# Performance work log

Hardware: AMD Instinct MI355X
Metric: run time of the kernel (lower is better)

The kernel has to match this reference:

```python
import jax, jax.numpy as jnp
import numpy as np

B, N, C, H, W = 2, 2048, 1024, 16, 8  # batch, seq, dim, heads, band half-width
HD = C // H
SCALE = HD ** -0.5


def band_mask(n, w):
    # rows i: allowed cols lo..hi inclusive, matching get_attn_mask
    i = jnp.arange(n)[:, None]
    j = jnp.arange(n)[None, :]
    lo = jnp.where(i <= w, 0, i - w)
    hi = jnp.where(n - i <= w, n - 1, i + w)
    return (j >= lo) & (j <= hi)  # [N, N] bool


def setup_inputs() -> dict:
    key = jax.random.key(0)
    k1, k2, k3 = jax.random.split(key, 3)
    x = jax.random.normal(k1, (B, N, C), dtype=jnp.float32)
    Wqkv = jax.random.normal(k2, (C, 3 * C), dtype=jnp.float32) * (C ** -0.5)
    Wproj = jax.random.normal(k3, (C, C), dtype=jnp.float32) * (C ** -0.5)
    bproj = jnp.zeros((C,), dtype=jnp.float32)
    return {"x": x, "Wqkv": Wqkv, "Wproj": Wproj, "bproj": bproj}


def reference(x, Wqkv, Wproj, bproj):
    b, n, c = x.shape
    qkv = (x @ Wqkv).reshape(b, n, 3, H, HD)
    qkv = jnp.transpose(qkv, (2, 0, 3, 1, 4))  # [3, B, H, N, HD]
    q, k, v = qkv[0], qkv[1], qkv[2]
    attn = jnp.einsum('bhqd,bhkd->bhqk', q, k) * SCALE
    mask = band_mask(n, W)  # [N, N]
    attn = jnp.where(mask[None, None], attn, jnp.float32(-1e9))
    attn = jax.nn.softmax(attn, axis=-1)
    # dropout omitted (eval mode / deterministic reference)
    out = jnp.einsum('bhqk,bhkd->bhqd', attn, v)
    out = jnp.transpose(out, (0, 2, 1, 3)).reshape(b, n, c)
    return out @ Wproj + bproj
```

## Files before the change

### kernel.cpp

```cpp
#include <hip/hip_runtime.h>

typedef unsigned short ushort_t;
typedef unsigned int uint32;

typedef __bf16 bf16x8 __attribute__((ext_vector_type(8)));
typedef float f32x4 __attribute__((ext_vector_type(4)));

__device__ __forceinline__ uint32 f2bf1(float f) {
  uint32 b = __float_as_uint(f);
  return (b + 0x7FFFu + ((b >> 16) & 1u)) >> 16;
}
__device__ __forceinline__ uint32 packbf2(float a, float b) {
  return f2bf1(a) | (f2bf1(b) << 16);
}
__device__ __forceinline__ float bflo(uint32 u) { return __uint_as_float(u << 16); }
__device__ __forceinline__ float bfhi(uint32 u) { return __uint_as_float(u & 0xFFFF0000u); }

__device__ __forceinline__ void gload16(const void* g, void* l) {
  __builtin_amdgcn_global_load_lds(
      (const __attribute__((address_space(1))) unsigned int*)g,
      (__attribute__((address_space(3))) unsigned int*)l, 16, 0, 0);
}

__global__ __launch_bounds__(256) void prep_inputs(
    const float* __restrict__ x, ushort_t* __restrict__ xb,
    const float* __restrict__ Wqkv, ushort_t* __restrict__ wqkvT,
    const float* __restrict__ Wproj, ushort_t* __restrict__ wprT) {
  int bx = blockIdx.x;
  const int tid = threadIdx.x;
  if (bx < 4096) {
    const int i = bx * 256 + tid;
    float4 v = ((const float4*)x)[i];
    uint2 r;
    r.x = packbf2(v.x, v.y);
    r.y = packbf2(v.z, v.w);
    ((uint2*)xb)[i] = r;
    return;
  }
  bx -= 4096;
  const int gx = bx & 127, gy = bx >> 7;
  __shared__ float tile[32][33];
  const int tx = tid & 31, ty = tid >> 5;
  const float* src;
  ushort_t* dst;
  int Cc, c0;
  if (gx < 96) { src = Wqkv;  dst = wqkvT; Cc = 3072; c0 = gx << 5; }
  else         { src = Wproj; dst = wprT;  Cc = 1024; c0 = (gx - 96) << 5; }
  const int r0 = gy << 5;
#pragma unroll
  for (int i = 0; i < 4; ++i)
    tile[ty + i * 8][tx] = src[(size_t)(r0 + ty + i * 8) * Cc + c0 + tx];
  __syncthreads();
#pragma unroll
  for (int i = 0; i < 4; ++i)
    dst[(size_t)(c0 + ty + i * 8) * 1024 + r0 + tx] = (ushort_t)f2bf1(tile[tx][ty + i * 8]);
}


template <int ROWS>
__device__ __forceinline__ void stage2(ushort_t* dst, const ushort_t* gbase,
                                       int ldK, int tid) {
  const int r = tid >> 2, s = tid & 3;
  const int c = ((s ^ ((r >> 1) & 3)) << 3);
  const int wvb = (tid >> 6) << 9;
  const ushort_t* g = gbase + (size_t)r * ldK + c;
  gload16(g, dst + wvb);
  if (ROWS == 128) gload16(g + (size_t)64 * ldK, dst + 2048 + wvb);
}

template <bool OUT_BF16, int MF, int NF>
__global__ __launch_bounds__(256) void gemm2p(
    const ushort_t* __restrict__ A, const ushort_t* __restrict__ Bt,
    void* __restrict__ Cout, const float* __restrict__ bias,
    const int M, const int Nn, const int K) {
  constexpr int BM = MF * 32, BN = NF * 32;
  constexpr int AL = BM * 32, BL = BN * 32;
  __shared__ ushort_t lA[2 * AL];
  __shared__ ushort_t lB[2 * BL];
  const int tid = threadIdx.x;
  const int lane = tid & 63, wave = tid >> 6;
  const int wm = wave >> 1, wn = wave & 1;

  const int nwg = gridDim.x * gridDim.y;
  const int wg0 = blockIdx.y * gridDim.x + blockIdx.x;
  const int q8 = nwg >> 3;
  const int wg = (wg0 & 7) * q8 + (wg0 >> 3);
  const int bm = (wg / gridDim.x) * BM;
  const int bn = (wg % gridDim.x) * BN;

  const int l15 = lane & 15, l16 = lane >> 4;
  const int cK = ((l16 ^ ((l15 >> 1) & 3)) << 3);

  const ushort_t* gA = A + (size_t)bm * K;
  const ushort_t* gB = Bt + (size_t)bn * K;

  f32x4 acc[MF][NF] = {};

  stage2<BM>(lA, gA, K, tid);
  stage2<BN>(lB, gB, K, tid);
  __syncthreads();

  int buf = 0;
  for (int k0 = 0; k0 < K; k0 += 32) {
    if (k0 + 32 < K) {
      stage2<BM>(lA + (buf ^ 1) * AL, gA + k0 + 32, K, tid);
      stage2<BN>(lB + (buf ^ 1) * BL, gB + k0 + 32, K, tid);
    }
    bf16x8 a[MF], b[NF];
#pragma unroll
    for (int m = 0; m < MF; ++m)
      a[m] = *(const bf16x8*)&lA[buf * AL + ((wm * MF + m) * 16 + l15) * 32 + cK];
#pragma unroll
    for (int n = 0; n < NF; ++n)
      b[n] = *(const bf16x8*)&lB[buf * BL + ((wn * NF + n) * 16 + l15) * 32 + cK];
#pragma unroll
    for (int m = 0; m < MF; ++m)
#pragma unroll
      for (int n = 0; n < NF; ++n)
        acc[m][n] = __builtin_amdgcn_mfma_f32_16x16x32_bf16(a[m], b[n], acc[m][n], 0, 0, 0);
    __syncthreads();
    buf ^= 1;
  }

  const int r0 = bm + wm * (MF * 16) + (l16 << 2);
  const int c0 = bn + wn * (NF * 16) + l15;
#pragma unroll
  for (int m = 0; m < MF; ++m)
#pragma unroll
    for (int n = 0; n < NF; ++n)
#pragma unroll
      for (int j = 0; j < 4; ++j) {
        const int row = r0 + m * 16 + j;
        const int col = c0 + n * 16;
        if (OUT_BF16)
          ((ushort_t*)Cout)[(size_t)row * Nn + col] = (ushort_t)f2bf1(acc[m][n][j]);
        else
          ((float*)Cout)[(size_t)row * Nn + col] = acc[m][n][j] + bias[col];
      }
}

__global__ __launch_bounds__(256) void attn_band(
    const ushort_t* __restrict__ qkv, ushort_t* __restrict__ aout) {
  __shared__ float Ks[80 * 68];
  __shared__ float Vs[80 * 68];
  const int tid = threadIdx.x;
  const int i0 = blockIdx.x << 6;
  const int h = blockIdx.y;
  const int b = blockIdx.z;
  const size_t rowbase = (size_t)b * 2048;

  for (int idx = tid; idx < 1280; idx += 256) {
    const int t = idx >> 4, c = idx & 15;
    const int j = i0 - 8 + t;
    float k0 = 0.f, k1 = 0.f, k2 = 0.f, k3 = 0.f;
    float v0 = 0.f, v1 = 0.f, v2 = 0.f, v3 = 0.f;
    if ((unsigned)j < 2048u) {
      const ushort_t* p = qkv + (rowbase + j) * 3072 + (h << 6) + (c << 2);
      uint2 rk = *(const uint2*)(p + 1024);
      uint2 rv = *(const uint2*)(p + 2048);
      k0 = bflo(rk.x); k1 = bfhi(rk.x); k2 = bflo(rk.y); k3 = bfhi(rk.y);
      v0 = bflo(rv.x); v1 = bfhi(rv.x); v2 = bflo(rv.y); v3 = bfhi(rv.y);
    }
    *(float4*)&Ks[t * 68 + (c << 2)] = make_float4(k0, k1, k2, k3);
    *(float4*)&Vs[t * 68 + (c << 2)] = make_float4(v0, v1, v2, v3);
  }
  __syncthreads();

  const int lane = tid & 63, wv = tid >> 6;
  const int qs = lane >> 2, dg = lane & 3;
  const int qi = (wv << 4) + qs;
  const int i = i0 + qi;

  const ushort_t* qp = qkv + (rowbase + i) * 3072 + (h << 6) + (dg << 4);
  float q[16];
  {
    uint4 u0 = *(const uint4*)qp;
    uint4 u1 = *(const uint4*)(qp + 8);
    q[0] = bflo(u0.x); q[1] = bfhi(u0.x); q[2] = bflo(u0.y); q[3] = bfhi(u0.y);
    q[4] = bflo(u0.z); q[5] = bfhi(u0.z); q[6] = bflo(u0.w); q[7] = bfhi(u0.w);
    q[8] = bflo(u1.x); q[9] = bfhi(u1.x); q[10] = bflo(u1.y); q[11] = bfhi(u1.y);
    q[12] = bflo(u1.z); q[13] = bfhi(u1.z); q[14] = bflo(u1.w); q[15] = bfhi(u1.w);
  }

  float s[17];
#pragma unroll
  for (int jo = 0; jo < 17; ++jo) {
    const float* kr = &Ks[(qi + jo) * 68 + (dg << 4)];
    float d = 0.f;
#pragma unroll
    for (int c = 0; c < 4; ++c) {
      float4 kv = *(const float4*)(kr + (c << 2));
      d += q[c * 4 + 0] * kv.x + q[c * 4 + 1] * kv.y +
           q[c * 4 + 2] * kv.z + q[c * 4 + 3] * kv.w;
    }
    d += __shfl_xor(d, 1);
    d += __shfl_xor(d, 2);
    const int jg = i - 8 + jo;
    s[jo] = ((unsigned)jg < 2048u) ? d * 0.125f : -1e30f;
  }
  float m = s[0];
#pragma unroll
  for (int jo = 1; jo < 17; ++jo) m = fmaxf(m, s[jo]);
  float sum = 0.f;
#pragma unroll
  for (int jo = 0; jo < 17; ++jo) {
    s[jo] = __expf(s[jo] - m);
    sum += s[jo];
  }
  const float inv = 1.f / sum;

  float o[16];
#pragma unroll
  for (int dd = 0; dd < 16; ++dd) o[dd] = 0.f;
#pragma unroll
  for (int jo = 0; jo < 17; ++jo) {
    const float* vr = &Vs[(qi + jo) * 68 + (dg << 4)];
    const float w = s[jo];
#pragma unroll
    for (int c = 0; c < 4; ++c) {
      float4 vv = *(const float4*)(vr + (c << 2));
      o[c * 4 + 0] += w * vv.x; o[c * 4 + 1] += w * vv.y;
      o[c * 4 + 2] += w * vv.z; o[c * 4 + 3] += w * vv.w;
    }
  }

  ushort_t* op = aout + (rowbase + i) * 1024 + (h << 6) + (dg << 4);
  uint4 w0, w1;
  w0.x = packbf2(o[0] * inv, o[1] * inv);
  w0.y = packbf2(o[2] * inv, o[3] * inv);
  w0.z = packbf2(o[4] * inv, o[5] * inv);
  w0.w = packbf2(o[6] * inv, o[7] * inv);
  w1.x = packbf2(o[8] * inv, o[9] * inv);
  w1.y = packbf2(o[10] * inv, o[11] * inv);
  w1.z = packbf2(o[12] * inv, o[13] * inv);
  w1.w = packbf2(o[14] * inv, o[15] * inv);
  *(uint4*)op = w0;
  *(uint4*)(op + 8) = w1;
}

extern "C" void kernel_launch(void* const* d_in, const int* in_sizes, int n_in,
                              void* d_out, int out_size, void* d_ws, size_t ws_size,
                              hipStream_t stream) {
  const float* x = (const float*)d_in[0];
  const float* Wqkv = (const float*)d_in[1];
  const float* Wproj = (const float*)d_in[2];
  const float* bproj = (const float*)d_in[3];
  float* out = (float*)d_out;

  char* ws = (char*)d_ws;
  ushort_t* xb    = (ushort_t*)(ws);
  ushort_t* wqkvT = (ushort_t*)(ws + (8u << 20));
  ushort_t* wprT  = (ushort_t*)(ws + (14u << 20));
  ushort_t* qkv   = (ushort_t*)(ws + (16u << 20));
  ushort_t* aoutb = (ushort_t*)(ws + (40u << 20));

  prep_inputs<<<8192, 256, 0, stream>>>(x, xb, Wqkv, wqkvT, Wproj, wprT);
  gemm2p<true, 4, 4><<<dim3(24, 32), 256, 0, stream>>>(
      xb, wqkvT, qkv, nullptr, 4096, 3072, 1024);
  attn_band<<<dim3(32, 16, 2), 256, 0, stream>>>(qkv, aoutb);
  gemm2p<false, 2, 4><<<dim3(8, 64), 256, 0, stream>>>(
      aoutb, wprT, out, bproj, 4096, 1024, 1024);
}
```

Baseline: 81.74 us.

## Fuse x fp32-to-bf16 conversion into QKV GEMM A-tile loading

Drops the separate x conversion pass and its bf16 buffer in the prep kernel. The QKV GEMM now reads fp32 x directly into registers, converts to bf16 and writes the tile into LDS after the MFMAs, in a software-pipelined way. This saves a full read/write round trip of x, but the GEMM now reads twice the A bytes per tile. It also loses the async global_load_lds path for A, which adds register pressure and VALU work.

Measured after the change: 89.04 us. 8.9% more time.

```diff
diff --git a/kernel.cpp b/kernel.cpp
--- a/kernel.cpp
+++ b/kernel.cpp
@@ -22,22 +22,11 @@
       (__attribute__((address_space(3))) unsigned int*)l, 16, 0, 0);
 }
 
-__global__ __launch_bounds__(256) void prep_inputs(
-    const float* __restrict__ x, ushort_t* __restrict__ xb,
+__global__ __launch_bounds__(256) void prep_weights(
     const float* __restrict__ Wqkv, ushort_t* __restrict__ wqkvT,
     const float* __restrict__ Wproj, ushort_t* __restrict__ wprT) {
-  int bx = blockIdx.x;
+  const int bx = blockIdx.x;
   const int tid = threadIdx.x;
-  if (bx < 4096) {
-    const int i = bx * 256 + tid;
-    float4 v = ((const float4*)x)[i];
-    uint2 r;
-    r.x = packbf2(v.x, v.y);
-    r.y = packbf2(v.z, v.w);
-    ((uint2*)xb)[i] = r;
-    return;
-  }
-  bx -= 4096;
   const int gx = bx & 127, gy = bx >> 7;
   __shared__ float tile[32][33];
   const int tx = tid & 31, ty = tid >> 5;
@@ -68,9 +57,9 @@
   if (ROWS == 128) gload16(g + (size_t)64 * ldK, dst + 2048 + wvb);
 }
 
-template <bool OUT_BF16, int MF, int NF>
+template <bool OUT_BF16, bool A_F32, int MF, int NF>
 __global__ __launch_bounds__(256) void gemm2p(
-    const ushort_t* __restrict__ A, const ushort_t* __restrict__ Bt,
+    const void* __restrict__ Av, const ushort_t* __restrict__ Bt,
     void* __restrict__ Cout, const float* __restrict__ bias,
     const int M, const int Nn, const int K) {
   constexpr int BM = MF * 32, BN = NF * 32;
@@ -91,19 +80,56 @@
   const int l15 = lane & 15, l16 = lane >> 4;
   const int cK = ((l16 ^ ((l15 >> 1) & 3)) << 3);
 
-  const ushort_t* gA = A + (size_t)bm * K;
+  const int sr = tid >> 2, ss = tid & 3;
+  const int sc = ((ss ^ ((sr >> 1) & 3)) << 3);
+  const int wvb = (tid >> 6) << 9;
+
+  const ushort_t* gA16 = A_F32 ? nullptr : (const ushort_t*)Av + (size_t)bm * K;
+  const float*    gA32 = A_F32 ? (const float*)Av + (size_t)bm * K : nullptr;
   const ushort_t* gB = Bt + (size_t)bn * K;
 
   f32x4 acc[MF][NF] = {};
 
-  stage2<BM>(lA, gA, K, tid);
+  if constexpr (A_F32) {
+    const float* g = gA32 + (size_t)sr * K + sc;
+    float4 u0 = *(const float4*)g;
+    float4 u1 = *(const float4*)(g + 4);
+    uint4 w;
+    w.x = packbf2(u0.x, u0.y); w.y = packbf2(u0.z, u0.w);
+    w.z = packbf2(u1.x, u1.y); w.w = packbf2(u1.z, u1.w);
+    *(uint4*)&lA[wvb + lane * 8] = w;
+    if (BM == 128) {
+      const float* g2 = g + (size_t)64 * K;
+      float4 v0 = *(const float4*)g2;
+      float4 v1 = *(const float4*)(g2 + 4);
+      uint4 w2;
+      w2.x = packbf2(v0.x, v0.y); w2.y = packbf2(v0.z, v0.w);
+      w2.z = packbf2(v1.x, v1.y); w2.w = packbf2(v1.z, v1.w);
+      *(uint4*)&lA[2048 + wvb + lane * 8] = w2;
+    }
+  } else {
+    stage2<BM>(lA, gA16, K, tid);
+  }
   stage2<BN>(lB, gB, K, tid);
   __syncthreads();
 
   int buf = 0;
   for (int k0 = 0; k0 < K; k0 += 32) {
-    if (k0 + 32 < K) {
-      stage2<BM>(lA + (buf ^ 1) * AL, gA + k0 + 32, K, tid);
+    const bool nk = (k0 + 32) < K;
+    float4 u0, u1, v0, v1;
+    if (nk) {
+      if constexpr (A_F32) {
+        const float* g = gA32 + (size_t)sr * K + k0 + 32 + sc;
+        u0 = *(const float4*)g;
+        u1 = *(const float4*)(g + 4);
+        if (BM == 128) {
+          const float* g2 = g + (size_t)64 * K;
+          v0 = *(const float4*)g2;
+          v1 = *(const float4*)(g2 + 4);
+        }
+      } else {
+        stage2<BM>(lA + (buf ^ 1) * AL, gA16 + k0 + 32, K, tid);
+      }
       stage2<BN>(lB + (buf ^ 1) * BL, gB + k0 + 32, K, tid);
     }
     bf16x8 a[MF], b[NF];
@@ -118,6 +144,21 @@
 #pragma unroll
       for (int n = 0; n < NF; ++n)
         acc[m][n] = __builtin_amdgcn_mfma_f32_16x16x32_bf16(a[m], b[n], acc[m][n], 0, 0, 0);
+    if (nk) {
+      if constexpr (A_F32) {
+        ushort_t* dst = lA + (buf ^ 1) * AL;
+        uint4 w;
+        w.x = packbf2(u0.x, u0.y); w.y = packbf2(u0.z, u0.w);
+        w.z = packbf2(u1.x, u1.y); w.w = packbf2(u1.z, u1.w);
+        *(uint4*)&dst[wvb + lane * 8] = w;
+        if (BM == 128) {
+          uint4 w2;
+          w2.x = packbf2(v0.x, v0.y); w2.y = packbf2(v0.z, v0.w);
+          w2.z = packbf2(v1.x, v1.y); w2.w = packbf2(v1.z, v1.w);
+          *(uint4*)&dst[2048 + wvb + lane * 8] = w2;
+        }
+      }
+    }
     __syncthreads();
     buf ^= 1;
   }
@@ -248,16 +289,15 @@
   float* out = (float*)d_out;
 
   char* ws = (char*)d_ws;
-  ushort_t* xb    = (ushort_t*)(ws);
   ushort_t* wqkvT = (ushort_t*)(ws + (8u << 20));
   ushort_t* wprT  = (ushort_t*)(ws + (14u << 20));
   ushort_t* qkv   = (ushort_t*)(ws + (16u << 20));
   ushort_t* aoutb = (ushort_t*)(ws + (40u << 20));
 
-  prep_inputs<<<8192, 256, 0, stream>>>(x, xb, Wqkv, wqkvT, Wproj, wprT);
-  gemm2p<true, 4, 4><<<dim3(24, 32), 256, 0, stream>>>(
-      xb, wqkvT, qkv, nullptr, 4096, 3072, 1024);
+  prep_weights<<<4096, 256, 0, stream>>>(Wqkv, wqkvT, Wproj, wprT);
+  gemm2p<true, true, 4, 4><<<dim3(24, 32), 256, 0, stream>>>(
+      x, wqkvT, qkv, nullptr, 4096, 3072, 1024);
   attn_band<<<dim3(32, 16, 2), 256, 0, stream>>>(qkv, aoutb);
-  gemm2p<false, 2, 4><<<dim3(8, 64), 256, 0, stream>>>(
+  gemm2p<false, false, 2, 4><<<dim3(8, 64), 256, 0, stream>>>(
       aoutb, wprT, out, bproj, 4096, 1024, 1024);
 }
```
